# Kernel tuning notes

Measured on AMD Instinct MI355X. Metric: run time of the kernel, lower is better.

Reference implementation:

```python
import jax, jax.numpy as jnp
import numpy as np

T, B, V, E, H, L = 70, 64, 10000, 512, 1024, 2


def setup_inputs() -> dict:
    key = jax.random.key(0)
    ks = jax.random.split(key, 10)
    k = float(1.0 / np.sqrt(H))
    u = lambda kk, shape, a: jax.random.uniform(kk, shape, jnp.float32, -a, a)
    return {
        "inputs": jax.random.randint(ks[0], (T, B), 0, V, dtype=jnp.int32),
        "hidden": jnp.zeros((L, B, H), jnp.float32),
        "emb_W": u(ks[1], (V, E), 0.1),
        "Wx0": u(ks[2], (H, E), k),   # nn.Linear weight is [out, in]
        "Wx1": u(ks[3], (H, H), k),
        "Wh0": u(ks[4], (H, H), k),
        "bh0": u(ks[5], (H,), k),
        "Wh1": u(ks[6], (H, H), k),
        "bh1": u(ks[7], (H,), k),
        "Wy": u(ks[8], (V, H), 0.1),
        "by": jnp.zeros((V,), jnp.float32),
    }


def reference(inputs, hidden, emb_W, Wx0, Wx1, Wh0, bh0, Wh1, bh1, Wy, by):
    # Stacked Elman RNN, dropout identity (dp_keep_prob=1.0).
    embedded = emb_W[inputs]  # [T, B, E]

    def step(h, x_t):
        # h: [L, B, H]; x_t: [B, E]
        h0 = jnp.tanh(x_t @ Wx0.T + h[0] @ Wh0.T + bh0)
        h1 = jnp.tanh(h0 @ Wx1.T + h[1] @ Wh1.T + bh1)
        new_h = jnp.stack([h0, h1])  # [L, B, H]
        logits_t = h1 @ Wy.T + by    # [B, V]
        return new_h, logits_t

    h_final, logits = jax.lax.scan(step, hidden, embedded)
    return logits, h_final  # [T, B, V], [L, B, H]
```

## Files before the change

### kernel.cpp

```cpp
#include <hip/hip_runtime.h>
#include <hip/hip_bf16.h>
#include <cmath>
#include <cstdint>


using u16 = unsigned short;
using u32 = unsigned int;
using u64 = unsigned long long;
typedef __attribute__((ext_vector_type(8))) short short8;
typedef __attribute__((ext_vector_type(4))) float f32x4;

#define MFMA_BF16(a, b, c) __builtin_amdgcn_mfma_f32_16x16x32_bf16((a), (b), (c), 0, 0, 0)

__device__ __forceinline__ u16 bf16_rne(float x) {
    u32 u = __float_as_uint(x);
    u32 r = u + 0x7FFFu + ((u >> 16) & 1u);
    return (u16)(r >> 16);
}
__device__ __forceinline__ float bf16_f(u16 h) {
    return __uint_as_float(((u32)h) << 16);
}
__device__ __forceinline__ void split2(float x, u16& hi, u16& lo) {
    hi = bf16_rne(x);
    lo = bf16_rne(x - bf16_f(hi));
}
__device__ __forceinline__ u64 pack4(u16 a, u16 b, u16 c, u16 d) {
    return (u64)a | ((u64)b << 16) | ((u64)c << 32) | ((u64)d << 48);
}

__device__ __forceinline__ void wait_count(int* f, int target) {
    if (threadIdx.x == 0) {
        while (__hip_atomic_load(f, __ATOMIC_RELAXED, __HIP_MEMORY_SCOPE_AGENT) < target)
            __builtin_amdgcn_s_sleep(1);
    }
    __syncthreads();
}
__device__ __forceinline__ void signal_done(int* f) {
    __syncthreads();
    if (threadIdx.x == 0)
        __hip_atomic_fetch_add(f, 1, __ATOMIC_RELAXED, __HIP_MEMORY_SCOPE_AGENT);
}

struct SplitSeg { const float* src; u16* hi; u16* lo; int n4; };

__global__ __launch_bounds__(256) void split_all_kernel(
    const float* __restrict__ Wx0, u16* Wx0h, u16* Wx0l,
    const float* __restrict__ Wx1, u16* Wx1h, u16* Wx1l,
    const float* __restrict__ Wh0, u16* Wh0h, u16* Wh0l,
    const float* __restrict__ Wh1, u16* Wh1h, u16* Wh1l,
    const float* __restrict__ Wy,  u16* Wyh,  u16* Wyl,
    const float* __restrict__ hid, u16* hsh,  u16* hsl)
{
    const int n0 = 131072;
    const int n1 = 262144;
    const int n2 = 262144;
    const int n3 = 262144;
    const int n4s = 2560000;
    const int n5 = 32768;
    int g = blockIdx.x * 256 + threadIdx.x;
    const float* src; u16* hi; u16* lo; int off;
    if      (g < n0)                       { src=Wx0; hi=Wx0h; lo=Wx0l; off=g; }
    else if ((g -= n0) < n1)               { src=Wx1; hi=Wx1h; lo=Wx1l; off=g; }
    else if ((g -= n1) < n2)               { src=Wh0; hi=Wh0h; lo=Wh0l; off=g; }
    else if ((g -= n2) < n3)               { src=Wh1; hi=Wh1h; lo=Wh1l; off=g; }
    else if ((g -= n3) < n4s)              { src=Wy;  hi=Wyh;  lo=Wyl;  off=g; }
    else if ((g -= n4s) < n5)              { src=hid; hi=hsh;  lo=hsl;  off=g; }
    else return;
    float4 v = *reinterpret_cast<const float4*>(src + (size_t)off * 4);
    u16 h0,h1,h2,h3,l0,l1,l2,l3;
    split2(v.x,h0,l0); split2(v.y,h1,l1); split2(v.z,h2,l2); split2(v.w,h3,l3);
    ushort4 H = {h0,h1,h2,h3}, L = {l0,l1,l2,l3};
    *reinterpret_cast<ushort4*>(hi + (size_t)off * 4) = H;
    *reinterpret_cast<ushort4*>(lo + (size_t)off * 4) = L;
}

__global__ __launch_bounds__(256) void gather_split_kernel(
    const float* __restrict__ emb, const int* __restrict__ idx,
    u16* __restrict__ hi, u16* __restrict__ lo, int n4)
{
    int g = blockIdx.x * 256 + threadIdx.x;
    if (g >= n4) return;
    int m  = g >> 7;
    int c4 = g & 127;
    const float* src = emb + (size_t)idx[m] * 512 + c4 * 4;
    float4 v = *reinterpret_cast<const float4*>(src);
    u16 h0,h1,h2,h3,l0,l1,l2,l3;
    split2(v.x,h0,l0); split2(v.y,h1,l1); split2(v.z,h2,l2); split2(v.w,h3,l3);
    ushort4 H = {h0,h1,h2,h3}, L = {l0,l1,l2,l3};
    size_t o = (size_t)m * 512 + c4 * 4;
    *reinterpret_cast<ushort4*>(hi + o) = H;
    *reinterpret_cast<ushort4*>(lo + o) = L;
}

__device__ __forceinline__ void gemm_tile(
    const u16* __restrict__ Ah, const u16* __restrict__ Al,
    const u16* __restrict__ Bh, const u16* __restrict__ Bl,
    const float* __restrict__ bias, float* __restrict__ C,
    int N, int K, int m0, int n0,
    u16* sAh, u16* sAl, u16* sBh, u16* sBl)
{
    const int tid  = threadIdx.x;
    const int lane = tid & 63;
    const int w    = tid >> 6;
    const int wr   = w >> 1, wc = w & 1;

    f32x4 acc[4][4];
    #pragma unroll
    for (int i = 0; i < 4; ++i)
        #pragma unroll
        for (int j = 0; j < 4; ++j) acc[i][j] = 0.0f;

    for (int k0 = 0; k0 < K; k0 += 32) {
        #pragma unroll
        for (int r = 0; r < 2; ++r) {
            int s   = r * 256 + tid;
            int row = s >> 2, q = s & 3;
            int gq  = q ^ (row & 3);
            int l16 = row * 32 + q * 8;
            size_t ga = (size_t)(m0 + row) * K + k0 + gq * 8;
            int brow = n0 + row; if (brow >= N) brow = N - 1;
            size_t gb = (size_t)brow * K + k0 + gq * 8;
            *reinterpret_cast<int4*>(sAh + l16) = *reinterpret_cast<const int4*>(Ah + ga);
            *reinterpret_cast<int4*>(sAl + l16) = *reinterpret_cast<const int4*>(Al + ga);
            *reinterpret_cast<int4*>(sBh + l16) = *reinterpret_cast<const int4*>(Bh + gb);
            *reinterpret_cast<int4*>(sBl + l16) = *reinterpret_cast<const int4*>(Bl + gb);
        }
        __syncthreads();

        const int q4 = lane >> 4;
        short8 afh[4], afl[4];
        #pragma unroll
        for (int i = 0; i < 4; ++i) {
            int ra  = wr * 64 + i * 16 + (lane & 15);
            int off = ra * 32 + (q4 ^ (ra & 3)) * 8;
            afh[i] = *reinterpret_cast<const short8*>(sAh + off);
            afl[i] = *reinterpret_cast<const short8*>(sAl + off);
        }
        #pragma unroll
        for (int j = 0; j < 4; ++j) {
            int rb  = wc * 64 + j * 16 + (lane & 15);
            int off = rb * 32 + (q4 ^ (rb & 3)) * 8;
            short8 bfh = *reinterpret_cast<const short8*>(sBh + off);
            short8 bfl = *reinterpret_cast<const short8*>(sBl + off);
            #pragma unroll
            for (int i = 0; i < 4; ++i) {
                acc[i][j] = MFMA_BF16(afh[i], bfh, acc[i][j]);
                acc[i][j] = MFMA_BF16(afh[i], bfl, acc[i][j]);
                acc[i][j] = MFMA_BF16(afl[i], bfh, acc[i][j]);
            }
        }
        __syncthreads();
    }

    #pragma unroll
    for (int j = 0; j < 4; ++j) {
        int n = n0 + wc * 64 + j * 16 + (lane & 15);
        if (n < N) {
            float bv = bias[n];
            #pragma unroll
            for (int i = 0; i < 4; ++i) {
                #pragma unroll
                for (int r = 0; r < 4; ++r) {
                    int m = m0 + wr * 64 + i * 16 + (lane >> 4) * 4 + r;
                    C[(size_t)m * N + n] = acc[i][j][r] + bv;
                }
            }
        }
    }
}

__global__ __launch_bounds__(256) void gemm_mfma(
    const u16* __restrict__ Ah, const u16* __restrict__ Al,
    const u16* __restrict__ Bh, const u16* __restrict__ Bl,
    const float* __restrict__ bias, float* __restrict__ C,
    int M, int N, int K)
{
    __shared__ u16 sAh[128*32], sAl[128*32], sBh[128*32], sBl[128*32];
    gemm_tile(Ah, Al, Bh, Bl, bias, C, N, K,
              blockIdx.y * 128, blockIdx.x * 128, sAh, sAl, sBh, sBl);
}

__global__ __launch_bounds__(256) void gemm_mfma_swz(
    const u16* __restrict__ Ah, const u16* __restrict__ Al,
    const u16* __restrict__ Bh, const u16* __restrict__ Bl,
    const float* __restrict__ bias, float* __restrict__ C,
    int M, int N, int K)
{
    __shared__ u16 sAh[128*32], sAl[128*32], sBh[128*32], sBl[128*32];
    const int NTN = 79;
    const int nwg = 35 * 79;
    const int q = nwg / 8, r = nwg % 8;
    int orig = (int)blockIdx.x;
    int xcd  = orig % 8;
    int idx  = orig / 8;
    int wg   = (xcd < r) ? (xcd * (q + 1) + idx)
                         : (r * (q + 1) + (xcd - r) * q + idx);
    int mb = wg / NTN, nb = wg % NTN;
    gemm_tile(Ah, Al, Bh, Bl, bias, C, N, K,
              mb * 128, nb * 128, sAh, sAl, sBh, sBl);
}

__global__ __launch_bounds__(256, 1) void rnn_persist2(
    const float* __restrict__ A0,
    const u16* __restrict__ hs0h, const u16* __restrict__ hs0l,
    const u16* __restrict__ hs1h, const u16* __restrict__ hs1l,
    u16* __restrict__ H0h, u16* __restrict__ H0l,
    u16* __restrict__ H1h, u16* __restrict__ H1l,
    const u16* __restrict__ Wh0h, const u16* __restrict__ Wh0l,
    const u16* __restrict__ Wx1h, const u16* __restrict__ Wx1l,
    const u16* __restrict__ Wh1h, const u16* __restrict__ Wh1l,
    const float* __restrict__ bh1, int* flags)
{
    __shared__ u16 sW[65536];
    __shared__ float sStage[64 * 17];
    const int tid   = threadIdx.x;
    const int lane  = tid & 63;
    const int w     = tid >> 6;
    const int layer = blockIdx.x >> 6;
    const int n0    = (int)(blockIdx.x & 63) * 16;
    const int m0    = w * 16;
    const int rb    = lane & 15;
    const int q4    = lane >> 4;
    const int arow  = m0 + rb;
    const size_t BH = 65536;
    const int srow  = tid >> 2;
    const int sc4   = (tid & 3) * 4;

    if (layer == 0) {
        for (int i = 0; i < 16; ++i) {
            int s    = i * 256 + tid;
            int arr  = s >> 11;
            int r    = (s >> 7) & 15;
            int g    = s & 127;
            int slot = g ^ (r & 7);
            const u16* src = (arr ? Wh0l : Wh0h) + (size_t)(n0 + r) * 1024 + g * 8;
            *reinterpret_cast<int4*>(sW + arr * 16384 + r * 1024 + slot * 8) =
                *reinterpret_cast<const int4*>(src);
        }
    } else {
        for (int i = 0; i < 32; ++i) {
            int s    = i * 256 + tid;
            int arr  = s >> 12;
            int r    = (s >> 8) & 15;
            int g    = s & 255;
            int slot = g ^ (r & 7);
            const u16* src;
            if (g < 128) src = (arr ? Wx1l : Wx1h) + (size_t)(n0 + r) * 1024 + g * 8;
            else         src = (arr ? Wh1l : Wh1h) + (size_t)(n0 + r) * 1024 + (g - 128) * 8;
            *reinterpret_cast<int4*>(sW + arr * 32768 + r * 2048 + slot * 8) =
                *reinterpret_cast<const int4*>(src);
        }
    }
    __syncthreads();

    if (layer == 0) {
        for (int t = 0; t < 70; ++t) {
            if (t > 0) wait_count(flags + (t - 1), 64);
            const u16* hph = t ? H0h + (size_t)(t - 1) * BH : hs0h;
            const u16* hpl = t ? H0l + (size_t)(t - 1) * BH : hs0l;
            f32x4 acc = {0.f, 0.f, 0.f, 0.f};
            #pragma unroll 8
            for (int kt = 0; kt < 32; ++kt) {
                short8 ah = *reinterpret_cast<const short8*>(hph + (size_t)arow * 1024 + kt * 32 + q4 * 8);
                short8 al = *reinterpret_cast<const short8*>(hpl + (size_t)arow * 1024 + kt * 32 + q4 * 8);
                int slot = (kt * 4 + q4) ^ (rb & 7);
                short8 bh = *reinterpret_cast<const short8*>(sW + rb * 1024 + slot * 8);
                short8 bl = *reinterpret_cast<const short8*>(sW + 16384 + rb * 1024 + slot * 8);
                acc = MFMA_BF16(ah, bh, acc);
                acc = MFMA_BF16(ah, bl, acc);
                acc = MFMA_BF16(al, bh, acc);
            }
            #pragma unroll
            for (int r = 0; r < 4; ++r) {
                int m = m0 + q4 * 4 + r;
                size_t o = (size_t)t * BH + (size_t)m * 1024 + n0 + rb;
                sStage[m * 17 + rb] = tanhf(acc[r] + A0[o]);
            }
            __syncthreads();
            {
                float f0 = sStage[srow * 17 + sc4 + 0];
                float f1 = sStage[srow * 17 + sc4 + 1];
                float f2 = sStage[srow * 17 + sc4 + 2];
                float f3 = sStage[srow * 17 + sc4 + 3];
                u16 a,b,c,d, la,lb,lc,ld;
                split2(f0,a,la); split2(f1,b,lb); split2(f2,c,lc); split2(f3,d,ld);
                size_t o64 = ((size_t)t * BH + (size_t)srow * 1024 + n0 + sc4) >> 2;
                __hip_atomic_store((u64*)H0h + o64, pack4(a,b,c,d),
                                   __ATOMIC_RELAXED, __HIP_MEMORY_SCOPE_AGENT);
                __hip_atomic_store((u64*)H0l + o64, pack4(la,lb,lc,ld),
                                   __ATOMIC_RELAXED, __HIP_MEMORY_SCOPE_AGENT);
            }
            signal_done(flags + t);
        }
    } else {
        for (int t = 0; t < 70; ++t) {
            wait_count(flags + t, 64);
            if (t > 0) wait_count(flags + 70 + (t - 1), 64);
            const u16* h0h  = H0h + (size_t)t * BH;
            const u16* h0l  = H0l + (size_t)t * BH;
            const u16* h1ph = t ? H1h + (size_t)(t - 1) * BH : hs1h;
            const u16* h1pl = t ? H1l + (size_t)(t - 1) * BH : hs1l;
            f32x4 acc = {0.f, 0.f, 0.f, 0.f};
            #pragma unroll 8
            for (int kt = 0; kt < 32; ++kt) {
                short8 ah = *reinterpret_cast<const short8*>(h0h + (size_t)arow * 1024 + kt * 32 + q4 * 8);
                short8 al = *reinterpret_cast<const short8*>(h0l + (size_t)arow * 1024 + kt * 32 + q4 * 8);
                int slot = (kt * 4 + q4) ^ (rb & 7);
                short8 bh = *reinterpret_cast<const short8*>(sW + rb * 2048 + slot * 8);
                short8 bl = *reinterpret_cast<const short8*>(sW + 32768 + rb * 2048 + slot * 8);
                acc = MFMA_BF16(ah, bh, acc);
                acc = MFMA_BF16(ah, bl, acc);
                acc = MFMA_BF16(al, bh, acc);
            }
            #pragma unroll 8
            for (int kt = 32; kt < 64; ++kt) {
                int ko = (kt - 32) * 32;
                short8 ah = *reinterpret_cast<const short8*>(h1ph + (size_t)arow * 1024 + ko + q4 * 8);
                short8 al = *reinterpret_cast<const short8*>(h1pl + (size_t)arow * 1024 + ko + q4 * 8);
                int slot = (kt * 4 + q4) ^ (rb & 7);
                short8 bh = *reinterpret_cast<const short8*>(sW + rb * 2048 + slot * 8);
                short8 bl = *reinterpret_cast<const short8*>(sW + 32768 + rb * 2048 + slot * 8);
                acc = MFMA_BF16(ah, bh, acc);
                acc = MFMA_BF16(ah, bl, acc);
                acc = MFMA_BF16(al, bh, acc);
            }
            const int n = n0 + rb;
            #pragma unroll
            for (int r = 0; r < 4; ++r) {
                int m = m0 + q4 * 4 + r;
                sStage[m * 17 + rb] = tanhf(acc[r] + bh1[n]);
            }
            __syncthreads();
            {
                float f0 = sStage[srow * 17 + sc4 + 0];
                float f1 = sStage[srow * 17 + sc4 + 1];
                float f2 = sStage[srow * 17 + sc4 + 2];
                float f3 = sStage[srow * 17 + sc4 + 3];
                u16 a,b,c,d, la,lb,lc,ld;
                split2(f0,a,la); split2(f1,b,lb); split2(f2,c,lc); split2(f3,d,ld);
                size_t o64 = ((size_t)t * BH + (size_t)srow * 1024 + n0 + sc4) >> 2;
                __hip_atomic_store((u64*)H1h + o64, pack4(a,b,c,d),
                                   __ATOMIC_RELAXED, __HIP_MEMORY_SCOPE_AGENT);
                __hip_atomic_store((u64*)H1l + o64, pack4(la,lb,lc,ld),
                                   __ATOMIC_RELAXED, __HIP_MEMORY_SCOPE_AGENT);
            }
            signal_done(flags + 70 + t);
        }
    }
}

__global__ __launch_bounds__(256) void hfinal_kernel(
    const u16* __restrict__ H0h, const u16* __restrict__ H0l,
    const u16* __restrict__ H1h, const u16* __restrict__ H1l,
    float* __restrict__ outp)
{
    int i = blockIdx.x * 256 + threadIdx.x;
    outp[i]         = bf16_f(H0h[i]) + bf16_f(H0l[i]);
    outp[65536 + i] = bf16_f(H1h[i]) + bf16_f(H1l[i]);
}

extern "C" void kernel_launch(void* const* d_in, const int* in_sizes, int n_in,
                              void* d_out, int out_size, void* d_ws, size_t ws_size,
                              hipStream_t stream)
{
    const int*   inputs = (const int*)  d_in[0];
    const float* hidden = (const float*)d_in[1];
    const float* embW   = (const float*)d_in[2];
    const float* Wx0    = (const float*)d_in[3];
    const float* Wx1    = (const float*)d_in[4];
    const float* Wh0    = (const float*)d_in[5];
    const float* bh0    = (const float*)d_in[6];
    const float* Wh1    = (const float*)d_in[7];
    const float* bh1    = (const float*)d_in[8];
    const float* Wy     = (const float*)d_in[9];
    const float* by     = (const float*)d_in[10];
    float* out = (float*)d_out;

    const int T = 70, B = 64, V = 10000, E = 512, H = 1024;
    const int M = T * B;
    const size_t MH = (size_t)M * H;
    const size_t BH = (size_t)B * H;

    char* wsb = (char*)d_ws;
    u16*   Wyh  = (u16*)(wsb);
    u16*   Wyl  = Wyh + (size_t)V * H;
    float* buf0 = (float*)(wsb + 40960000);
    u16*   H0h  = (u16*)(wsb + 59310080);
    u16*   H0l  = H0h + MH;
    u16*   H1h  = H0l + MH;
    u16*   H1l  = H1h + MH;
    u16*   Wx0h = H1l + MH;
    u16*   Wx0l = Wx0h + (size_t)H * E;
    u16*   Wx1h = Wx0l + (size_t)H * E;
    u16*   Wx1l = Wx1h + (size_t)H * H;
    u16*   Wh0h = Wx1l + (size_t)H * H;
    u16*   Wh0l = Wh0h + (size_t)H * H;
    u16*   Wh1h = Wh0l + (size_t)H * H;
    u16*   Wh1l = Wh1h + (size_t)H * H;
    u16*   hs0h = Wh1l + (size_t)H * H;
    u16*   hs0l = hs0h + BH;
    u16*   hs1h = hs0l + BH;
    u16*   hs1l = hs1h + BH;

    u16*   Agh   = (u16*)((char*)d_out + 20971520);
    u16*   Agl   = Agh + (size_t)M * E;
    int*   flags = (int*)((char*)d_out + 104857600);

    dim3 blk(256);

    hipMemsetAsync(flags, 0, 140 * sizeof(int), stream);

    split_all_kernel<<<dim3(13713), blk, 0, stream>>>(
        Wx0, Wx0h, Wx0l,
        Wx1, Wx1h, Wx1l,
        Wh0, Wh0h, Wh0l,
        Wh1, Wh1h, Wh1l,
        Wy,  Wyh,  Wyl,
        hidden, hs0h, hs0l);
    gather_split_kernel<<<dim3((M*E)/1024), blk, 0, stream>>>(embW, inputs, Agh, Agl, (M*E)/4);

    gemm_mfma<<<dim3(H/128, M/128), blk, 0, stream>>>(
        Agh, Agl, Wx0h, Wx0l, bh0, buf0, M, H, E);

    {
        const float* A0p = buf0;
        void* args[] = {
            (void*)&A0p,
            (void*)&hs0h, (void*)&hs0l, (void*)&hs1h, (void*)&hs1l,
            (void*)&H0h,  (void*)&H0l,  (void*)&H1h,  (void*)&H1l,
            (void*)&Wh0h, (void*)&Wh0l, (void*)&Wx1h, (void*)&Wx1l,
            (void*)&Wh1h, (void*)&Wh1l, (void*)&bh1, (void*)&flags
        };
        hipLaunchCooperativeKernel(reinterpret_cast<void*>(rnn_persist2),
                                   dim3(128), blk, args, 0, stream);
    }

    hfinal_kernel<<<dim3(256), blk, 0, stream>>>(
        H0h + (size_t)(T-1) * BH, H0l + (size_t)(T-1) * BH,
        H1h + (size_t)(T-1) * BH, H1l + (size_t)(T-1) * BH,
        out + (size_t)M * V);

    gemm_mfma_swz<<<dim3(35 * 79), blk, 0, stream>>>(
        H1h, H1l, Wyh, Wyl, by, out, M, V, H);
}
```

Measured before the change: 1.537 ms.

## Overlap output projection GEMM with RNN recurrence inside persistent kernel

Folds the final vocabulary projection GEMM into the persistent cooperative RNN kernel. 128 extra worker blocks each wait on per-timestep layer-1 completion flags and compute 128x128 logits tiles while the recurrence continues. Layer-1 signalling gains a release fence so workers see the hidden states, and A-tile loads use atomic agent-scope loads to avoid stale cache data. The change removes a separate serial GEMM launch, but the worker blocks compete with the recurrence for CUs and bandwidth, which could slow the latency-bound RNN steps. The flag buffer is also moved to the workspace and zeroed later.

After: 1.557 ms. Within noise of the previous version (+1.3%).

```diff
diff --git a/kernel.cpp b/kernel.cpp
--- a/kernel.cpp
+++ b/kernel.cpp
@@ -40,8 +40,13 @@
     if (threadIdx.x == 0)
         __hip_atomic_fetch_add(f, 1, __ATOMIC_RELAXED, __HIP_MEMORY_SCOPE_AGENT);
 }
-
-struct SplitSeg { const float* src; u16* hi; u16* lo; int n4; };
+__device__ __forceinline__ void signal_done_rel(int* f) {
+    __syncthreads();
+    if (threadIdx.x == 0) {
+        __builtin_amdgcn_fence(__ATOMIC_RELEASE, "agent");
+        __hip_atomic_fetch_add(f, 1, __ATOMIC_RELAXED, __HIP_MEMORY_SCOPE_AGENT);
+    }
+}
 
 __global__ __launch_bounds__(256) void split_all_kernel(
     const float* __restrict__ Wx0, u16* Wx0h, u16* Wx0l,
@@ -169,6 +174,95 @@
     }
 }
 
+__device__ __forceinline__ void gemm_tile_llcA(
+    const u16* __restrict__ Ah, const u16* __restrict__ Al,
+    const u16* __restrict__ Bh, const u16* __restrict__ Bl,
+    const float* __restrict__ bias, float* __restrict__ C,
+    int N, int K, int m0, int n0,
+    u16* sAh, u16* sAl, u16* sBh, u16* sBl)
+{
+    const int tid  = threadIdx.x;
+    const int lane = tid & 63;
+    const int w    = tid >> 6;
+    const int wr   = w >> 1, wc = w & 1;
+
+    f32x4 acc[4][4];
+    #pragma unroll
+    for (int i = 0; i < 4; ++i)
+        #pragma unroll
+        for (int j = 0; j < 4; ++j) acc[i][j] = 0.0f;
+
+    for (int k0 = 0; k0 < K; k0 += 32) {
+        #pragma unroll
+        for (int rr = 0; rr < 4; ++rr) {
+            int u2  = rr * 256 + tid;
+            int row = u2 >> 3, j = u2 & 7, q = j >> 1, hf = j & 1;
+            int gq  = q ^ (row & 3);
+            size_t ga = (size_t)(m0 + row) * K + k0 + gq * 8 + hf * 4;
+            u64 vh = __hip_atomic_load((const u64*)(Ah + ga),
+                                       __ATOMIC_RELAXED, __HIP_MEMORY_SCOPE_AGENT);
+            u64 vl = __hip_atomic_load((const u64*)(Al + ga),
+                                       __ATOMIC_RELAXED, __HIP_MEMORY_SCOPE_AGENT);
+            int l16 = row * 32 + q * 8 + hf * 4;
+            *reinterpret_cast<u64*>(sAh + l16) = vh;
+            *reinterpret_cast<u64*>(sAl + l16) = vl;
+        }
+        #pragma unroll
+        for (int r = 0; r < 2; ++r) {
+            int s   = r * 256 + tid;
+            int row = s >> 2, q = s & 3;
+            int gq  = q ^ (row & 3);
+            int brow = n0 + row; if (brow >= N) brow = N - 1;
+            size_t gb = (size_t)brow * K + k0 + gq * 8;
+            *reinterpret_cast<int4*>(sBh + row * 32 + q * 8) =
+                *reinterpret_cast<const int4*>(Bh + gb);
+            *reinterpret_cast<int4*>(sBl + row * 32 + q * 8) =
+                *reinterpret_cast<const int4*>(Bl + gb);
+        }
+        __syncthreads();
+
+        const int q4 = lane >> 4;
+        short8 afh[4], afl[4];
+        #pragma unroll
+        for (int i = 0; i < 4; ++i) {
+            int ra  = wr * 64 + i * 16 + (lane & 15);
+            int off = ra * 32 + (q4 ^ (ra & 3)) * 8;
+            afh[i] = *reinterpret_cast<const short8*>(sAh + off);
+            afl[i] = *reinterpret_cast<const short8*>(sAl + off);
+        }
+        #pragma unroll
+        for (int j = 0; j < 4; ++j) {
+            int rb  = wc * 64 + j * 16 + (lane & 15);
+            int off = rb * 32 + (q4 ^ (rb & 3)) * 8;
+            short8 bfh = *reinterpret_cast<const short8*>(sBh + off);
+            short8 bfl = *reinterpret_cast<const short8*>(sBl + off);
+            #pragma unroll
+            for (int i = 0; i < 4; ++i) {
+                acc[i][j] = MFMA_BF16(afh[i], bfh, acc[i][j]);
+                acc[i][j] = MFMA_BF16(afh[i], bfl, acc[i][j]);
+                acc[i][j] = MFMA_BF16(afl[i], bfh, acc[i][j]);
+            }
+        }
+        __syncthreads();
+    }
+
+    #pragma unroll
+    for (int j = 0; j < 4; ++j) {
+        int n = n0 + wc * 64 + j * 16 + (lane & 15);
+        if (n < N) {
+            float bv = bias[n];
+            #pragma unroll
+            for (int i = 0; i < 4; ++i) {
+                #pragma unroll
+                for (int r = 0; r < 4; ++r) {
+                    int m = m0 + wr * 64 + i * 16 + (lane >> 4) * 4 + r;
+                    C[(size_t)m * N + n] = acc[i][j][r] + bv;
+                }
+            }
+        }
+    }
+}
+
 __global__ __launch_bounds__(256) void gemm_mfma(
     const u16* __restrict__ Ah, const u16* __restrict__ Al,
     const u16* __restrict__ Bh, const u16* __restrict__ Bl,
@@ -180,27 +274,7 @@
               blockIdx.y * 128, blockIdx.x * 128, sAh, sAl, sBh, sBl);
 }
 
-__global__ __launch_bounds__(256) void gemm_mfma_swz(
-    const u16* __restrict__ Ah, const u16* __restrict__ Al,
-    const u16* __restrict__ Bh, const u16* __restrict__ Bl,
-    const float* __restrict__ bias, float* __restrict__ C,
-    int M, int N, int K)
-{
-    __shared__ u16 sAh[128*32], sAl[128*32], sBh[128*32], sBl[128*32];
-    const int NTN = 79;
-    const int nwg = 35 * 79;
-    const int q = nwg / 8, r = nwg % 8;
-    int orig = (int)blockIdx.x;
-    int xcd  = orig % 8;
-    int idx  = orig / 8;
-    int wg   = (xcd < r) ? (xcd * (q + 1) + idx)
-                         : (r * (q + 1) + (xcd - r) * q + idx);
-    int mb = wg / NTN, nb = wg % NTN;
-    gemm_tile(Ah, Al, Bh, Bl, bias, C, N, K,
-              mb * 128, nb * 128, sAh, sAl, sBh, sBl);
-}
-
-__global__ __launch_bounds__(256, 1) void rnn_persist2(
+__global__ __launch_bounds__(256, 1) void rnn_persist5(
     const float* __restrict__ A0,
     const u16* __restrict__ hs0h, const u16* __restrict__ hs0l,
     const u16* __restrict__ hs1h, const u16* __restrict__ hs1l,
@@ -209,20 +283,40 @@
     const u16* __restrict__ Wh0h, const u16* __restrict__ Wh0l,
     const u16* __restrict__ Wx1h, const u16* __restrict__ Wx1l,
     const u16* __restrict__ Wh1h, const u16* __restrict__ Wh1l,
-    const float* __restrict__ bh1, int* flags)
+    const float* __restrict__ bh1, int* flags,
+    const u16* __restrict__ Wyh, const u16* __restrict__ Wyl,
+    const float* __restrict__ by, float* __restrict__ Cout)
 {
     __shared__ u16 sW[65536];
     __shared__ float sStage[64 * 17];
     const int tid   = threadIdx.x;
     const int lane  = tid & 63;
     const int w     = tid >> 6;
+    const size_t BH = 65536;
+
+    if (blockIdx.x >= 128) {
+        int wkr = (int)blockIdx.x - 128;
+        u16* sAh = sW;
+        u16* sAl = sW + 4096;
+        u16* sBh = sW + 8192;
+        u16* sBl = sW + 12288;
+        const int NT = 35 * 79;
+        for (int tile = wkr; tile < NT; tile += 128) {
+            int mb = tile / 79, nb = tile % 79;
+            int t_hi = 2 * mb + 1;
+            wait_count(flags + 70 + t_hi, 64);
+            gemm_tile_llcA(H1h, H1l, Wyh, Wyl, by, Cout, 10000, 1024,
+                           mb * 128, nb * 128, sAh, sAl, sBh, sBl);
+        }
+        return;
+    }
+
     const int layer = blockIdx.x >> 6;
     const int n0    = (int)(blockIdx.x & 63) * 16;
     const int m0    = w * 16;
     const int rb    = lane & 15;
     const int q4    = lane >> 4;
     const int arow  = m0 + rb;
-    const size_t BH = 65536;
     const int srow  = tid >> 2;
     const int sc4   = (tid & 3) * 4;
 
@@ -344,7 +438,7 @@
                 __hip_atomic_store((u64*)H1l + o64, pack4(la,lb,lc,ld),
                                    __ATOMIC_RELAXED, __HIP_MEMORY_SCOPE_AGENT);
             }
-            signal_done(flags + 70 + t);
+            signal_done_rel(flags + 70 + t);
         }
     }
 }
@@ -401,26 +495,22 @@
     u16*   hs0l = hs0h + BH;
     u16*   hs1h = hs0l + BH;
     u16*   hs1l = hs1h + BH;
+    int*   flags = (int*)(wsb + 97058816);
 
     u16*   Agh   = (u16*)((char*)d_out + 20971520);
     u16*   Agl   = Agh + (size_t)M * E;
-    int*   flags = (int*)((char*)d_out + 104857600);
 
     dim3 blk(256);
 
-    hipMemsetAsync(flags, 0, 140 * sizeof(int), stream);
-
     split_all_kernel<<<dim3(13713), blk, 0, stream>>>(
-        Wx0, Wx0h, Wx0l,
-        Wx1, Wx1h, Wx1l,
-        Wh0, Wh0h, Wh0l,
-        Wh1, Wh1h, Wh1l,
-        Wy,  Wyh,  Wyl,
-        hidden, hs0h, hs0l);
+        Wx0, Wx0h, Wx0l, Wx1, Wx1h, Wx1l, Wh0, Wh0h, Wh0l,
+        Wh1, Wh1h, Wh1l, Wy, Wyh, Wyl, hidden, hs0h, hs0l);
     gather_split_kernel<<<dim3((M*E)/1024), blk, 0, stream>>>(embW, inputs, Agh, Agl, (M*E)/4);
 
     gemm_mfma<<<dim3(H/128, M/128), blk, 0, stream>>>(
         Agh, Agl, Wx0h, Wx0l, bh0, buf0, M, H, E);
+
+    hipMemsetAsync(flags, 0, 140 * sizeof(int), stream);
 
     {
         const float* A0p = buf0;
@@ -429,17 +519,15 @@
             (void*)&hs0h, (void*)&hs0l, (void*)&hs1h, (void*)&hs1l,
             (void*)&H0h,  (void*)&H0l,  (void*)&H1h,  (void*)&H1l,
             (void*)&Wh0h, (void*)&Wh0l, (void*)&Wx1h, (void*)&Wx1l,
-            (void*)&Wh1h, (void*)&Wh1l, (void*)&bh1, (void*)&flags
+            (void*)&Wh1h, (void*)&Wh1l, (void*)&bh1, (void*)&flags,
+            (void*)&Wyh, (void*)&Wyl, (void*)&by, (void*)&out
         };
-        hipLaunchCooperativeKernel(reinterpret_cast<void*>(rnn_persist2),
-                                   dim3(128), blk, args, 0, stream);
+        hipLaunchCooperativeKernel(reinterpret_cast<void*>(rnn_persist5),
+                                   dim3(256), blk, args, 0, stream);
     }
 
     hfinal_kernel<<<dim3(256), blk, 0, stream>>>(
         H0h + (size_t)(T-1) * BH, H0l + (size_t)(T-1) * BH,
         H1h + (size_t)(T-1) * BH, H1l + (size_t)(T-1) * BH,
         out + (size_t)M * V);
-
-    gemm_mfma_swz<<<dim3(35 * 79), blk, 0, stream>>>(
-        H1h, H1l, Wyh, Wyl, by, out, M, V, H);
-}
+}
```
